# Kernel optimization log

Hardware: AMD Instinct MI355X
Metric: run time of the kernel (lower is better)

## Reference

```python
import jax, jax.numpy as jnp
import numpy as np

VOLRADIUS = 256.0
DT = 1.0 / VOLRADIUS  # self.dt = dt / volradius with dt=1.0
N_STEPS = 64
B, H, W, K, M = 1, 256, 256, 64, 16


def setup_inputs() -> dict:
    rng = np.random.default_rng(0)
    # orthographic-ish ray bundle looking down +z through the primitive cloud
    ys, xs = np.meshgrid(np.linspace(-1., 1., H, dtype=np.float32),
                         np.linspace(-1., 1., W, dtype=np.float32), indexing='ij')
    raypos = np.broadcast_to(np.stack([xs, ys, np.full_like(xs, -0.125)], -1)[None],
                             (B, H, W, 3)).astype(np.float32).copy()
    raydir = np.zeros((B, H, W, 3), np.float32); raydir[..., 2] = 1.0
    tmin = np.zeros((B, H, W), np.float32)
    tminmax = np.stack([tmin, tmin + N_STEPS * DT], -1).astype(np.float32)
    # primpos is in WORLD units (module divides by volradius)
    primpos = rng.uniform(-0.1 * VOLRADIUS, 0.1 * VOLRADIUS, (B, K, 3)).astype(np.float32)
    q, _ = np.linalg.qr(rng.normal(size=(B, K, 3, 3)))
    primrot = q.astype(np.float32)
    primscale = rng.uniform(8., 16., (B, K, 3)).astype(np.float32)  # inverse half-extent
    primrgba = rng.uniform(0., 1., (B, K, 4, M, M, M)).astype(np.float32)
    return {
        'raypos': jnp.asarray(raypos), 'raydir': jnp.asarray(raydir),
        'tminmax': jnp.asarray(tminmax), 'primpos': jnp.asarray(primpos),
        'primrot': jnp.asarray(primrot), 'primscale': jnproundtrip(primscale) if False else jnp.asarray(primscale),
        'primrgba': jnp.asarray(primrgba),
    }


def _trilinear_sum(template, pos, primpos, primrot, primscale):
    # template [K,4,M,M,M]; pos [R,3]; returns summed rgba over primitives [R,4]
    Mv = template.shape[-1]
    kidx = jnp.arange(template.shape[0])[None, :]                      # [1,K]
    rel = pos[:, None, :] - primpos[None, :, :]                        # [R,K,3]
    # local = primscale * (primrot^T @ rel), inside prim iff |local| < 1
    local = jnp.einsum('kij,rki->rkj', primrot, rel) * primscale[None]  # [R,K,3]
    inside = jnp.all(jnp.abs(local) < 1.0, axis=-1)                    # [R,K]
    g = jnp.clip((local + 1.0) * 0.5 * (Mv - 1), 0.0, Mv - 1 - 1e-5)    # voxel coords (x,y,z)
    i0 = jnp.clip(jnp.floor(g).astype(jnp.int32), 0, Mv - 2)
    f = g - i0.astype(g.dtype)
    x0, y0, z0 = i0[..., 0], i0[..., 1], i0[..., 2]
    fx, fy, fz = f[..., 0], f[..., 1], f[..., 2]
    c = jnp.zeros(local.shape[:2] + (4,), template.dtype)
    for dz, wz in ((0, 1 - fz), (1, fz)):
        for dy, wy in ((0, 1 - fy), (1, fy)):
            for dx, wx in ((0, 1 - fx), (1, fx)):
                corner = template[kidx, :, z0 + dz, y0 + dy, x0 + dx]  # [R,K,4]
                c = c + corner * (wz * wy * wx)[..., None]
    c = c * inside[..., None]
    return c.sum(axis=1)                                               # [R,4]


def _march(raypos, raydir, tminmax, primpos, primrot, primscale, template):
    Hh, Ww, _ = raypos.shape
    R = Hh * Ww
    o = raypos.reshape(R, 3)
    d = raydir.reshape(R, 3)
    tmm = tminmax.reshape(R, 2)
    tmin, tmax = tmm[:, 0], tmm[:, 1]

    def step(carry, i):
        rgb, alpha = carry
        t = tmin + (i.astype(jnp.float32) + 0.5) * DT
        valid = t < tmax
        pos = o + t[:, None] * d
        s = _trilinear_sum(template, pos, primpos, primrot, primscale)  # [R,4]
        # MVP front-to-back saturating alpha compositing (early-term equivalent)
        contrib = jnp.minimum(1.0, alpha + s[:, 3] * DT) - alpha
        contrib = jnp.where(valid, contrib, 0.0)
        rgb = rgb + s[:, :3] * contrib[:, None]
        alpha = alpha + contrib
        return (rgb, alpha), None

    init = (jnp.zeros((R, 3), jnp.float32), jnp.zeros((R,), jnp.float32))
    (rgb, alpha), _ = jax.lax.scan(jax.checkpoint(step), init, jnp.arange(N_STEPS))
    return jnp.concatenate([rgb, alpha[:, None]], -1).reshape(Hh, Ww, 4)


def reference(raypos, raydir, tminmax, primpos, primrot, primscale, primrgba):
    primpos_n = primpos / VOLRADIUS  # module normalizes primpos by volume radius
    rayrgba = jax.vmap(_march)(raypos, raydir, tminmax, primpos_n, primrot, primscale, primrgba)
    rayrgba = jnp.transpose(rayrgba, (0, 3, 1, 2))  # [B,4,H,W]
    rayrgb = rayrgba[:, :3]
    rayalpha = rayrgba[:, 3:4]
    return rayrgb, rayalpha, rayrgba
```

## Files before the change

kernel.cpp:

```cpp
#include <hip/hip_runtime.h>
#include <hip/hip_fp16.h>

#define Rtot 65536
#define Wimg 256
#define Kp 64
#define NSTEPS 64
#define DTc (1.0f/256.0f)
#define INV_VOLR (1.0f/256.0f)
#define NITEMS 16384

#define PD_OFF    0u
#define TB_OFF    4096u
#define TT_OFF    65536u
#define SBUF_OFF  8388608u
#define WS_NEED   (SBUF_OFF + (size_t)NITEMS*256*8)

__device__ __forceinline__ unsigned int pack2(float a, float b) {
  __half2 h = __floats2half2_rn(a, b);
  return *(unsigned int*)&h;
}

__global__ __launch_bounds__(256) void setup_kernel(
    const float* __restrict__ raypos, const float* __restrict__ raydir,
    const float* __restrict__ tminmax, const float* __restrict__ primpos,
    const float* __restrict__ primrot, const float* __restrict__ primscale,
    const float* __restrict__ tmpl,
    float* __restrict__ tb, uint4* __restrict__ tth, float* __restrict__ pd) {
  int bid = blockIdx.x, tid = threadIdx.x;
  if (bid < 256) {
    __shared__ float smn[4][7], smx[4][7];
    int w = (bid & 15)*16 + (tid & 15);
    int h = (bid >> 4)*16 + (tid >> 4);
    int r = h*Wimg + w;
    float v[7];
    v[0] = raypos[r*3+0]; v[1] = raypos[r*3+1]; v[2] = raypos[r*3+2];
    v[3] = raydir[r*3+0]; v[4] = raydir[r*3+1]; v[5] = raydir[r*3+2];
    v[6] = tminmax[r*2+0];
    float mn[7], mx[7];
#pragma unroll
    for (int i = 0; i < 7; ++i) { mn[i] = v[i]; mx[i] = v[i]; }
#pragma unroll
    for (int m = 1; m < 64; m <<= 1) {
#pragma unroll
      for (int i = 0; i < 7; ++i) {
        mn[i] = fminf(mn[i], __shfl_xor(mn[i], m));
        mx[i] = fmaxf(mx[i], __shfl_xor(mx[i], m));
      }
    }
    int wv = tid >> 6;
    if ((tid & 63) == 0) {
#pragma unroll
      for (int i = 0; i < 7; ++i) { smn[wv][i] = mn[i]; smx[wv][i] = mx[i]; }
    }
    __syncthreads();
    if (tid == 0) {
#pragma unroll
      for (int i = 0; i < 7; ++i) {
        tb[bid*16 + i]     = fminf(fminf(smn[0][i], smn[1][i]), fminf(smn[2][i], smn[3][i]));
        tb[bid*16 + 8 + i] = fmaxf(fmaxf(smx[0][i], smx[1][i]), fmaxf(smx[2][i], smx[3][i]));
      }
    }
  } else if (bid < 320) {
    int k = bid - 256;
    const float* b0 = tmpl + (((size_t)k) << 14);
    uint4* o = tth + (k << 12);
    for (int v = tid; v < 4096; v += 256) {
      int x = v & 15;
      int xn = (x < 15) ? v + 1 : v;
      uint4 q;
      q.x = pack2(b0[v],       b0[4096+v]);
      q.y = pack2(b0[8192+v],  b0[12288+v]);
      q.z = pack2(b0[xn],      b0[4096+xn]);
      q.w = pack2(b0[8192+xn], b0[12288+xn]);
      o[v] = q;
    }
  } else {
    int k = tid;
    if (k < Kp) {
      float sc0 = primscale[k*3+0], sc1 = primscale[k*3+1], sc2 = primscale[k*3+2];
      float* o = pd + (k << 4);
      o[0] = primpos[k*3+0] * INV_VOLR;
      o[1] = primpos[k*3+1] * INV_VOLR;
      o[2] = primpos[k*3+2] * INV_VOLR;
      o[3] = 0.0f; o[4] = 0.0f; o[5] = 0.0f;
#pragma unroll
      for (int i = 0; i < 3; ++i) {
        o[6+i*3+0] = primrot[k*9+i*3+0]*sc0;
        o[6+i*3+1] = primrot[k*9+i*3+1]*sc1;
        o[6+i*3+2] = primrot[k*9+i*3+2]*sc2;
      }
      o[15] = 0.0f;
    }
  }
}

__global__ __launch_bounds__(256) void shade_kernel(
    const float* __restrict__ raypos, const float* __restrict__ raydir,
    const float* __restrict__ tminmax, const float* __restrict__ pd,
    const float* __restrict__ tb, const uint4* __restrict__ tth,
    uint2* __restrict__ sbuf) {
  __shared__ int s_list[Kp];
  __shared__ int s_cnt;
  int item = blockIdx.x;
  int tile = item >> 6, step = item & 63;
  int tid = threadIdx.x;
  if (tid < 64) {
    const float* t0 = tb + tile*16;
    float cst = ((float)step + 0.5f)*DTc;
    float tl = t0[6] + cst, th = t0[14] + cst;
    const float* p = pd + (tid << 4);
    float rlo[3], rhi[3];
#pragma unroll
    for (int a = 0; a < 3; ++a) {
      float ol = t0[a], oh = t0[8+a], dl = t0[3+a], dh = t0[11+a];
      float p1 = tl*dl, p2 = tl*dh, p3 = th*dl, p4 = th*dh;
      float lo = ol + fminf(fminf(p1, p2), fminf(p3, p4));
      float hi = oh + fmaxf(fmaxf(p1, p2), fmaxf(p3, p4));
      rlo[a] = lo - p[a];
      rhi[a] = hi - p[a];
    }
    bool pass = true;
#pragma unroll
    for (int j = 0; j < 3; ++j) {
      float llo = 0.f, lhi = 0.f;
#pragma unroll
      for (int a = 0; a < 3; ++a) {
        float rsc = p[6+a*3+j];
        float q1 = rlo[a]*rsc, q2 = rhi[a]*rsc;
        llo += fminf(q1, q2);
        lhi += fmaxf(q1, q2);
      }
      pass = pass && (llo < 1.0f) && (lhi > -1.0f);
    }
    unsigned long long mask = __ballot(pass);
    if (tid == 0) s_cnt = (int)__popcll(mask);
    if (pass) {
      int pos = (int)__popcll(mask & ((1ull << tid) - 1ull));
      s_list[pos] = tid;
    }
  }
  __syncthreads();
  int cnt = s_cnt;
  if (cnt == 0) return;

  int w = (tile & 15)*16 + (tid & 15);
  int h = (tile >> 4)*16 + (tid >> 4);
  int r = h*Wimg + w;
  float t = tminmax[r*2] + ((float)step + 0.5f)*DTc;
  float px = fmaf(t, raydir[r*3+0], raypos[r*3+0]);
  float py = fmaf(t, raydir[r*3+1], raypos[r*3+1]);
  float pz = fmaf(t, raydir[r*3+2], raypos[r*3+2]);
  float c0 = 0.f, c1 = 0.f, c2 = 0.f, c3 = 0.f;
  for (int j = 0; j < cnt; ++j) {
    int k = __builtin_amdgcn_readfirstlane(s_list[j]);
    const float* p = pd + (k << 4);
    float relx = px - p[0], rely = py - p[1], relz = pz - p[2];
    float lx = relx*p[6] + rely*p[9]  + relz*p[12];
    float ly = relx*p[7] + rely*p[10] + relz*p[13];
    float lz = relx*p[8] + rely*p[11] + relz*p[14];
    bool inside = fabsf(lx) < 1.0f && fabsf(ly) < 1.0f && fabsf(lz) < 1.0f;
    if (__any(inside)) {
      if (inside) {
        float gx = fminf(fmaxf((lx + 1.0f)*7.5f, 0.0f), 14.99999f);
        float gy = fminf(fmaxf((ly + 1.0f)*7.5f, 0.0f), 14.99999f);
        float gz = fminf(fmaxf((lz + 1.0f)*7.5f, 0.0f), 14.99999f);
        int ix = (int)gx, iy = (int)gy, iz = (int)gz;
        ix = ix > 14 ? 14 : ix; iy = iy > 14 ? 14 : iy; iz = iz > 14 ? 14 : iz;
        float fx = gx - (float)ix, fy = gy - (float)iy, fz = gz - (float)iz;
        float wx0 = 1.0f - fx, wy0 = 1.0f - fy, wz0 = 1.0f - fz;
        float w00 = wz0*wy0, w01 = wz0*fy, w10 = fz*wy0, w11 = fz*fy;
        const uint4* tb4 = tth + ((size_t)k << 12) + iz*256 + iy*16 + ix;
        uint4 q00 = tb4[0];
        uint4 q01 = tb4[16];
        uint4 q10 = tb4[256];
        uint4 q11 = tb4[272];
#define ACCQ(q, wv) { \
        float2 p01 = __half22float2(*(const __half2*)&q.x); \
        float2 p23 = __half22float2(*(const __half2*)&q.y); \
        float2 n01 = __half22float2(*(const __half2*)&q.z); \
        float2 n23 = __half22float2(*(const __half2*)&q.w); \
        float wa = (wv)*wx0, wb = (wv)*fx; \
        c0 = fmaf(p01.x, wa, fmaf(n01.x, wb, c0)); \
        c1 = fmaf(p01.y, wa, fmaf(n01.y, wb, c1)); \
        c2 = fmaf(p23.x, wa, fmaf(n23.x, wb, c2)); \
        c3 = fmaf(p23.y, wa, fmaf(n23.y, wb, c3)); }
        ACCQ(q00, w00) ACCQ(q01, w01) ACCQ(q10, w10) ACCQ(q11, w11)
#undef ACCQ
      }
    }
  }
  __half2 lo2 = __floats2half2_rn(c0, c1);
  __half2 hi2 = __floats2half2_rn(c2, c3);
  sbuf[item*256 + tid] = make_uint2(*(unsigned int*)&lo2, *(unsigned int*)&hi2);
}

__global__ __launch_bounds__(256) void composite_kernel(
    const float* __restrict__ tminmax, const uint2* __restrict__ sbuf,
    float* __restrict__ out) {
  int tid = threadIdx.x;
  int b = blockIdx.x;
  int w = (b & 15)*16 + (tid & 15);
  int h = (b >> 4)*16 + (tid >> 4);
  int r = h*Wimg + w;
  float tmin = tminmax[r*2+0], tmax = tminmax[r*2+1];
  float rgb0 = 0.f, rgb1 = 0.f, rgb2 = 0.f, alpha = 0.f;
#pragma unroll
  for (int i = 0; i < NSTEPS; ++i) {
    uint2 pk = sbuf[(b*NSTEPS + i)*256 + tid];
    float2 lf = __half22float2(*(__half2*)&pk.x);
    float2 hf = __half22float2(*(__half2*)&pk.y);
    float t = tmin + ((float)i + 0.5f)*DTc;
    float contrib = fminf(1.0f, fmaf(hf.y, DTc, alpha)) - alpha;
    contrib = (t < tmax) ? contrib : 0.0f;
    rgb0 = fmaf(lf.x, contrib, rgb0);
    rgb1 = fmaf(lf.y, contrib, rgb1);
    rgb2 = fmaf(hf.x, contrib, rgb2);
    alpha += contrib;
  }
  out[0*Rtot + r] = rgb0;
  out[1*Rtot + r] = rgb1;
  out[2*Rtot + r] = rgb2;
  out[3*Rtot + r] = alpha;
  out[4*Rtot + r] = rgb0;
  out[5*Rtot + r] = rgb1;
  out[6*Rtot + r] = rgb2;
  out[7*Rtot + r] = alpha;
}

__global__ __launch_bounds__(256) void fallback_kernel(
    const float* __restrict__ raypos, const float* __restrict__ raydir,
    const float* __restrict__ tminmax,
    const float* __restrict__ primpos, const float* __restrict__ primrot,
    const float* __restrict__ primscale, const float* __restrict__ tmpl,
    float* __restrict__ out) {
  __shared__ float s_pd[Kp][16];
  int tx = threadIdx.x, ty = threadIdx.y;
  int tid = ty*16 + tx;
  if (tid < Kp) {
    int k = tid;
    float sc0 = primscale[k*3+0], sc1 = primscale[k*3+1], sc2 = primscale[k*3+2];
    s_pd[k][0] = primpos[k*3+0]*INV_VOLR;
    s_pd[k][1] = primpos[k*3+1]*INV_VOLR;
    s_pd[k][2] = primpos[k*3+2]*INV_VOLR;
#pragma unroll
    for (int i = 0; i < 3; ++i) {
      s_pd[k][6+i*3+0] = primrot[k*9+i*3+0]*sc0;
      s_pd[k][6+i*3+1] = primrot[k*9+i*3+1]*sc1;
      s_pd[k][6+i*3+2] = primrot[k*9+i*3+2]*sc2;
    }
  }
  __syncthreads();
  int w = blockIdx.x*16 + tx, h = blockIdx.y*16 + ty;
  int r = h*Wimg + w;
  float ox = raypos[r*3+0], oy = raypos[r*3+1], oz = raypos[r*3+2];
  float dx = raydir[r*3+0], dy = raydir[r*3+1], dz = raydir[r*3+2];
  float tmin = tminmax[r*2+0], tmax = tminmax[r*2+1];
  float rgb0=0.f, rgb1=0.f, rgb2=0.f, alpha=0.f;
  for (int i = 0; i < NSTEPS; ++i) {
    float t = tmin + ((float)i + 0.5f)*DTc;
    float px = fmaf(t, dx, ox), py = fmaf(t, dy, oy), pz = fmaf(t, dz, oz);
    float c[4] = {0.f, 0.f, 0.f, 0.f};
    for (int k = 0; k < Kp; ++k) {
      const float* p = &s_pd[k][0];
      float relx = px - p[0], rely = py - p[1], relz = pz - p[2];
      float lx = relx*p[6] + rely*p[9]  + relz*p[12];
      float ly = relx*p[7] + rely*p[10] + relz*p[13];
      float lz = relx*p[8] + rely*p[11] + relz*p[14];
      if (!(fabsf(lx) < 1.0f && fabsf(ly) < 1.0f && fabsf(lz) < 1.0f)) continue;
      float gx = fminf(fmaxf((lx + 1.0f)*7.5f, 0.0f), 14.99999f);
      float gy = fminf(fmaxf((ly + 1.0f)*7.5f, 0.0f), 14.99999f);
      float gz = fminf(fmaxf((lz + 1.0f)*7.5f, 0.0f), 14.99999f);
      int ix = (int)gx, iy = (int)gy, iz = (int)gz;
      ix = ix > 14 ? 14 : ix; iy = iy > 14 ? 14 : iy; iz = iz > 14 ? 14 : iz;
      float fx = gx - (float)ix, fy = gy - (float)iy, fz = gz - (float)iz;
      float wx0 = 1.0f - fx, wy0 = 1.0f - fy, wz0 = 1.0f - fz;
      float w00 = wz0*wy0, w01 = wz0*fy, w10 = fz*wy0, w11 = fz*fy;
      const float* base = tmpl + (((size_t)k) << 14) + iz*256 + iy*16 + ix;
#pragma unroll
      for (int ch = 0; ch < 4; ++ch) {
        const float* bb = base + ch*4096;
        c[ch] += (bb[0]  *wx0 + bb[1]  *fx) * w00
               + (bb[16] *wx0 + bb[17] *fx) * w01
               + (bb[256]*wx0 + bb[257]*fx) * w10
               + (bb[272]*wx0 + bb[273]*fx) * w11;
      }
    }
    float contrib = fminf(1.0f, fmaf(c[3], DTc, alpha)) - alpha;
    contrib = (t < tmax) ? contrib : 0.0f;
    rgb0 = fmaf(c[0], contrib, rgb0);
    rgb1 = fmaf(c[1], contrib, rgb1);
    rgb2 = fmaf(c[2], contrib, rgb2);
    alpha += contrib;
  }
  out[0*Rtot + r] = rgb0;
  out[1*Rtot + r] = rgb1;
  out[2*Rtot + r] = rgb2;
  out[3*Rtot + r] = alpha;
  out[4*Rtot + r] = rgb0;
  out[5*Rtot + r] = rgb1;
  out[6*Rtot + r] = rgb2;
  out[7*Rtot + r] = alpha;
}

extern "C" void kernel_launch(void* const* d_in, const int* in_sizes, int n_in,
                              void* d_out, int out_size, void* d_ws, size_t ws_size,
                              hipStream_t stream) {
  const float* raypos    = (const float*)d_in[0];
  const float* raydir    = (const float*)d_in[1];
  const float* tminmax   = (const float*)d_in[2];
  const float* primpos   = (const float*)d_in[3];
  const float* primrot   = (const float*)d_in[4];
  const float* primscale = (const float*)d_in[5];
  const float* primrgba  = (const float*)d_in[6];
  float* out = (float*)d_out;

  if (ws_size >= WS_NEED) {
    char* ws = (char*)d_ws;
    float* pd   = (float*)(ws + PD_OFF);
    float* tb   = (float*)(ws + TB_OFF);
    uint4* tth  = (uint4*)(ws + TT_OFF);
    uint2* sbuf = (uint2*)(ws + SBUF_OFF);

    hipMemsetAsync(sbuf, 0, (size_t)NITEMS*256*8, stream);
    setup_kernel<<<321, 256, 0, stream>>>(raypos, raydir, tminmax, primpos,
                                          primrot, primscale, primrgba,
                                          tb, tth, pd);
    shade_kernel<<<NITEMS, 256, 0, stream>>>(raypos, raydir, tminmax, pd, tb,
                                             tth, sbuf);
    composite_kernel<<<256, 256, 0, stream>>>(tminmax, sbuf, out);
  } else {
    fallback_kernel<<<dim3(16,16), dim3(16,16), 0, stream>>>(
        raypos, raydir, tminmax, primpos, primrot, primscale, primrgba, out);
  }
}
```

Measured before the change: 70.38 us.

## Replace sbuf memset with per-item flags and pair primitive gathers

Drops the 32 MB hipMemsetAsync of the shading buffer. Each shade block now writes a per-(tile,step) occupancy flag, and the composite kernel skips reading sbuf for empty items. The shading loop is also restructured to process two primitives per iteration with branchless masked weights, so the gathers for both primitives are issued together. The trade-off is loads issued for lanes outside the primitive (weighted by zero), and extra register pressure.

```diff
diff --git a/kernel.cpp b/kernel.cpp
--- a/kernel.cpp
+++ b/kernel.cpp
@@ -11,6 +11,7 @@
 
 #define PD_OFF    0u
 #define TB_OFF    4096u
+#define FLAG_OFF  20480u
 #define TT_OFF    65536u
 #define SBUF_OFF  8388608u
 #define WS_NEED   (SBUF_OFF + (size_t)NITEMS*256*8)
@@ -94,11 +95,44 @@
   }
 }
 
+__device__ __forceinline__ void prim_setup(const float* __restrict__ p,
+    float px, float py, float pz, bool& inside, const uint4*& addr,
+    float& wx0, float& wfx, float& w00, float& w01, float& w10, float& w11,
+    const uint4* __restrict__ tth, int k) {
+  float relx = px - p[0], rely = py - p[1], relz = pz - p[2];
+  float lx = relx*p[6] + rely*p[9]  + relz*p[12];
+  float ly = relx*p[7] + rely*p[10] + relz*p[13];
+  float lz = relx*p[8] + rely*p[11] + relz*p[14];
+  inside = fabsf(lx) < 1.0f && fabsf(ly) < 1.0f && fabsf(lz) < 1.0f;
+  float gx = fminf(fmaxf((lx + 1.0f)*7.5f, 0.0f), 14.99999f);
+  float gy = fminf(fmaxf((ly + 1.0f)*7.5f, 0.0f), 14.99999f);
+  float gz = fminf(fmaxf((lz + 1.0f)*7.5f, 0.0f), 14.99999f);
+  int ix = (int)gx, iy = (int)gy, iz = (int)gz;
+  ix = ix > 14 ? 14 : ix; iy = iy > 14 ? 14 : iy; iz = iz > 14 ? 14 : iz;
+  float fx = gx - (float)ix, fy = gy - (float)iy, fz = gz - (float)iz;
+  float m = inside ? 1.0f : 0.0f;
+  wx0 = 1.0f - fx; wfx = fx;
+  float wy0 = 1.0f - fy, wz0 = 1.0f - fz;
+  w00 = wz0*wy0*m; w01 = wz0*fy*m; w10 = fz*wy0*m; w11 = fz*fy*m;
+  addr = tth + ((size_t)k << 12) + iz*256 + iy*16 + ix;
+}
+
+#define ACCQ(q, wv, wx0, wfx) { \
+  float2 p01 = __half22float2(*(const __half2*)&q.x); \
+  float2 p23 = __half22float2(*(const __half2*)&q.y); \
+  float2 n01 = __half22float2(*(const __half2*)&q.z); \
+  float2 n23 = __half22float2(*(const __half2*)&q.w); \
+  float wa = (wv)*(wx0), wb = (wv)*(wfx); \
+  c0 = fmaf(p01.x, wa, fmaf(n01.x, wb, c0)); \
+  c1 = fmaf(p01.y, wa, fmaf(n01.y, wb, c1)); \
+  c2 = fmaf(p23.x, wa, fmaf(n23.x, wb, c2)); \
+  c3 = fmaf(p23.y, wa, fmaf(n23.y, wb, c3)); }
+
 __global__ __launch_bounds__(256) void shade_kernel(
     const float* __restrict__ raypos, const float* __restrict__ raydir,
     const float* __restrict__ tminmax, const float* __restrict__ pd,
     const float* __restrict__ tb, const uint4* __restrict__ tth,
-    uint2* __restrict__ sbuf) {
+    uint2* __restrict__ sbuf, unsigned char* __restrict__ flags) {
   __shared__ int s_list[Kp];
   __shared__ int s_cnt;
   int item = blockIdx.x;
@@ -141,6 +175,7 @@
   }
   __syncthreads();
   int cnt = s_cnt;
+  if (tid == 0) flags[item] = (unsigned char)(cnt > 0 ? 1 : 0);
   if (cnt == 0) return;
 
   int w = (tile & 15)*16 + (tid & 15);
@@ -151,70 +186,68 @@
   float py = fmaf(t, raydir[r*3+1], raypos[r*3+1]);
   float pz = fmaf(t, raydir[r*3+2], raypos[r*3+2]);
   float c0 = 0.f, c1 = 0.f, c2 = 0.f, c3 = 0.f;
-  for (int j = 0; j < cnt; ++j) {
-    int k = __builtin_amdgcn_readfirstlane(s_list[j]);
-    const float* p = pd + (k << 4);
-    float relx = px - p[0], rely = py - p[1], relz = pz - p[2];
-    float lx = relx*p[6] + rely*p[9]  + relz*p[12];
-    float ly = relx*p[7] + rely*p[10] + relz*p[13];
-    float lz = relx*p[8] + rely*p[11] + relz*p[14];
-    bool inside = fabsf(lx) < 1.0f && fabsf(ly) < 1.0f && fabsf(lz) < 1.0f;
-    if (__any(inside)) {
-      if (inside) {
-        float gx = fminf(fmaxf((lx + 1.0f)*7.5f, 0.0f), 14.99999f);
-        float gy = fminf(fmaxf((ly + 1.0f)*7.5f, 0.0f), 14.99999f);
-        float gz = fminf(fmaxf((lz + 1.0f)*7.5f, 0.0f), 14.99999f);
-        int ix = (int)gx, iy = (int)gy, iz = (int)gz;
-        ix = ix > 14 ? 14 : ix; iy = iy > 14 ? 14 : iy; iz = iz > 14 ? 14 : iz;
-        float fx = gx - (float)ix, fy = gy - (float)iy, fz = gz - (float)iz;
-        float wx0 = 1.0f - fx, wy0 = 1.0f - fy, wz0 = 1.0f - fz;
-        float w00 = wz0*wy0, w01 = wz0*fy, w10 = fz*wy0, w11 = fz*fy;
-        const uint4* tb4 = tth + ((size_t)k << 12) + iz*256 + iy*16 + ix;
-        uint4 q00 = tb4[0];
-        uint4 q01 = tb4[16];
-        uint4 q10 = tb4[256];
-        uint4 q11 = tb4[272];
-#define ACCQ(q, wv) { \
-        float2 p01 = __half22float2(*(const __half2*)&q.x); \
-        float2 p23 = __half22float2(*(const __half2*)&q.y); \
-        float2 n01 = __half22float2(*(const __half2*)&q.z); \
-        float2 n23 = __half22float2(*(const __half2*)&q.w); \
-        float wa = (wv)*wx0, wb = (wv)*fx; \
-        c0 = fmaf(p01.x, wa, fmaf(n01.x, wb, c0)); \
-        c1 = fmaf(p01.y, wa, fmaf(n01.y, wb, c1)); \
-        c2 = fmaf(p23.x, wa, fmaf(n23.x, wb, c2)); \
-        c3 = fmaf(p23.y, wa, fmaf(n23.y, wb, c3)); }
-        ACCQ(q00, w00) ACCQ(q01, w01) ACCQ(q10, w10) ACCQ(q11, w11)
-#undef ACCQ
-      }
-    }
-  }
-  __half2 lo2 = __floats2half2_rn(c0, c1);
-  __half2 hi2 = __floats2half2_rn(c2, c3);
-  sbuf[item*256 + tid] = make_uint2(*(unsigned int*)&lo2, *(unsigned int*)&hi2);
+
+  int j = 0;
+  for (; j + 1 < cnt; j += 2) {
+    int k0 = __builtin_amdgcn_readfirstlane(s_list[j]);
+    int k1 = __builtin_amdgcn_readfirstlane(s_list[j+1]);
+    bool in0, in1;
+    const uint4 *a0, *a1;
+    float wx0a, wfxa, w00a, w01a, w10a, w11a;
+    float wx0b, wfxb, w00b, w01b, w10b, w11b;
+    prim_setup(pd + (k0 << 4), px, py, pz, in0, a0, wx0a, wfxa, w00a, w01a, w10a, w11a, tth, k0);
+    prim_setup(pd + (k1 << 4), px, py, pz, in1, a1, wx0b, wfxb, w00b, w01b, w10b, w11b, tth, k1);
+    if (__any(in0 || in1)) {
+      uint4 q00 = a0[0], q01 = a0[16], q10 = a0[256], q11 = a0[272];
+      uint4 r00 = a1[0], r01 = a1[16], r10 = a1[256], r11 = a1[272];
+      ACCQ(q00, w00a, wx0a, wfxa) ACCQ(q01, w01a, wx0a, wfxa)
+      ACCQ(q10, w10a, wx0a, wfxa) ACCQ(q11, w11a, wx0a, wfxa)
+      ACCQ(r00, w00b, wx0b, wfxb) ACCQ(r01, w01b, wx0b, wfxb)
+      ACCQ(r10, w10b, wx0b, wfxb) ACCQ(r11, w11b, wx0b, wfxb)
+    }
+  }
+  if (j < cnt) {
+    int k0 = __builtin_amdgcn_readfirstlane(s_list[j]);
+    bool in0;
+    const uint4* a0;
+    float wx0a, wfxa, w00a, w01a, w10a, w11a;
+    prim_setup(pd + (k0 << 4), px, py, pz, in0, a0, wx0a, wfxa, w00a, w01a, w10a, w11a, tth, k0);
+    if (__any(in0)) {
+      uint4 q00 = a0[0], q01 = a0[16], q10 = a0[256], q11 = a0[272];
+      ACCQ(q00, w00a, wx0a, wfxa) ACCQ(q01, w01a, wx0a, wfxa)
+      ACCQ(q10, w10a, wx0a, wfxa) ACCQ(q11, w11a, wx0a, wfxa)
+    }
+  }
+  sbuf[item*256 + tid] = make_uint2(pack2(c0, c1), pack2(c2, c3));
 }
 
 __global__ __launch_bounds__(256) void composite_kernel(
     const float* __restrict__ tminmax, const uint2* __restrict__ sbuf,
-    float* __restrict__ out) {
+    const unsigned char* __restrict__ flags, float* __restrict__ out) {
+  __shared__ unsigned char s_flags[NSTEPS];
   int tid = threadIdx.x;
   int b = blockIdx.x;
+  if (tid < NSTEPS) s_flags[tid] = flags[b*NSTEPS + tid];
+  __syncthreads();
   int w = (b & 15)*16 + (tid & 15);
   int h = (b >> 4)*16 + (tid >> 4);
   int r = h*Wimg + w;
   float tmin = tminmax[r*2+0], tmax = tminmax[r*2+1];
   float rgb0 = 0.f, rgb1 = 0.f, rgb2 = 0.f, alpha = 0.f;
-#pragma unroll
   for (int i = 0; i < NSTEPS; ++i) {
-    uint2 pk = sbuf[(b*NSTEPS + i)*256 + tid];
-    float2 lf = __half22float2(*(__half2*)&pk.x);
-    float2 hf = __half22float2(*(__half2*)&pk.y);
+    float s0 = 0.f, s1 = 0.f, s2 = 0.f, s3 = 0.f;
+    if (s_flags[i]) {
+      uint2 pk = sbuf[(b*NSTEPS + i)*256 + tid];
+      float2 lf = __half22float2(*(__half2*)&pk.x);
+      float2 hf = __half22float2(*(__half2*)&pk.y);
+      s0 = lf.x; s1 = lf.y; s2 = hf.x; s3 = hf.y;
+    }
     float t = tmin + ((float)i + 0.5f)*DTc;
-    float contrib = fminf(1.0f, fmaf(hf.y, DTc, alpha)) - alpha;
+    float contrib = fminf(1.0f, fmaf(s3, DTc, alpha)) - alpha;
     contrib = (t < tmax) ? contrib : 0.0f;
-    rgb0 = fmaf(lf.x, contrib, rgb0);
-    rgb1 = fmaf(lf.y, contrib, rgb1);
-    rgb2 = fmaf(hf.x, contrib, rgb2);
+    rgb0 = fmaf(s0, contrib, rgb0);
+    rgb1 = fmaf(s1, contrib, rgb1);
+    rgb2 = fmaf(s2, contrib, rgb2);
     alpha += contrib;
   }
   out[0*Rtot + r] = rgb0;
@@ -316,18 +349,18 @@
 
   if (ws_size >= WS_NEED) {
     char* ws = (char*)d_ws;
-    float* pd   = (float*)(ws + PD_OFF);
-    float* tb   = (float*)(ws + TB_OFF);
-    uint4* tth  = (uint4*)(ws + TT_OFF);
-    uint2* sbuf = (uint2*)(ws + SBUF_OFF);
-
-    hipMemsetAsync(sbuf, 0, (size_t)NITEMS*256*8, stream);
+    float* pd            = (float*)(ws + PD_OFF);
+    float* tb            = (float*)(ws + TB_OFF);
+    unsigned char* flags = (unsigned char*)(ws + FLAG_OFF);
+    uint4* tth           = (uint4*)(ws + TT_OFF);
+    uint2* sbuf          = (uint2*)(ws + SBUF_OFF);
+
     setup_kernel<<<321, 256, 0, stream>>>(raypos, raydir, tminmax, primpos,
                                           primrot, primscale, primrgba,
                                           tb, tth, pd);
     shade_kernel<<<NITEMS, 256, 0, stream>>>(raypos, raydir, tminmax, pd, tb,
-                                             tth, sbuf);
-    composite_kernel<<<256, 256, 0, stream>>>(tminmax, sbuf, out);
+                                             tth, sbuf, flags);
+    composite_kernel<<<256, 256, 0, stream>>>(tminmax, sbuf, flags, out);
   } else {
     fallback_kernel<<<dim3(16,16), dim3(16,16), 0, stream>>>(
         raypos, raydir, tminmax, primpos, primrot, primscale, primrgba, out);
```

Result: slower. 76.61 us (+8.9%).
